# Kernel optimization log

Hardware: AMD Instinct MI355X
Metric: run time of the kernel (lower is better)

Reference implementation:

```python
import jax, jax.numpy as jnp
import numpy as np

G = 20000          # num_genes
B = 256            # batch_size
NNZ = 640000       # sparse adjacency nonzeros (avg degree 32)
K = 2              # PPR iterations
ALPHA = 0.1
NUM_CLASS = 33


def _spmm(rows, cols, vals, x):
    # y = A @ x with A sparse COO [G, G], x dense [G, B]
    return jax.ops.segment_sum(vals[:, None] * x[cols], rows, num_segments=G)


def setup_inputs() -> dict:
    key = jax.random.key(0)
    ks = jax.random.split(key, 18)
    inp = {
        "x_sample": jax.random.normal(ks[0], (B * G,), jnp.float32),
        "x_TF": jax.random.normal(ks[1], (B * G,), jnp.float32),
        "adj_rows": jax.random.randint(ks[2], (NNZ,), 0, G, jnp.int32),
        "adj_cols": jax.random.randint(ks[3], (NNZ,), 0, G, jnp.int32),
        "adj_vals": jax.random.uniform(ks[4], (NNZ,), jnp.float32) / 32.0,
        "adjT_rows": jax.random.randint(ks[5], (NNZ,), 0, G, jnp.int32),
        "adjT_cols": jax.random.randint(ks[6], (NNZ,), 0, G, jnp.int32),
        "adjT_vals": jax.random.uniform(ks[7], (NNZ,), jnp.float32) / 32.0,
        # learned scalar affine params (torch.rand(1))
        "emb_mut": jax.random.uniform(ks[8], (1,), jnp.float32),
        "bias_mut": jax.random.uniform(ks[9], (1,), jnp.float32),
        "emb_exp": jax.random.uniform(ks[10], (1,), jnp.float32),
        "bias_exp": jax.random.uniform(ks[11], (1,), jnp.float32),
        # MLP params (torch Linear layout: W [out, in])
        "W1": jax.random.normal(ks[12], (1024, G), jnp.float32) * (1.0 / np.sqrt(G)),
        "b1": jnp.zeros((1024,), jnp.float32),
        "W2": jax.random.normal(ks[13], (128, 1024), jnp.float32) * (1.0 / 32.0),
        "b2": jnp.zeros((128,), jnp.float32),
        "W3": jax.random.normal(ks[14], (NUM_CLASS, 128), jnp.float32) * (1.0 / np.sqrt(128.0)),
        "b3": jnp.zeros((NUM_CLASS,), jnp.float32),
    }
    return inp


def reference(x_sample, x_TF, adj_rows, adj_cols, adj_vals,
              adjT_rows, adjT_cols, adjT_vals,
              emb_mut, bias_mut, emb_exp, bias_exp,
              W1, b1, W2, b2, W3, b3):
    # scalar affine embedding + relu
    emb_m = jax.nn.relu(emb_mut * x_sample + bias_mut)   # [B*G]
    emb_e = jax.nn.relu(emb_exp * x_TF + bias_exp)       # [B*G]
    xs = emb_m.reshape(B, G).T                            # [G, B]
    xt = emb_e.reshape(B, G).T                            # [G, B]
    hs, ht = xs, xt
    one_m_a = 1.0 - ALPHA
    for _ in range(K):
        xs = _spmm(adj_rows, adj_cols, adj_vals, one_m_a * xs)
        xt = _spmm(adjT_rows, adjT_cols, adjT_vals, one_m_a * xt)
    xs = xs + ALPHA * hs
    xt = xt + ALPHA * ht
    hadamard = (xs * xt).T                                # [B, G]
    h1 = jax.nn.relu(hadamard @ W1.T + b1)                # [B, 1024]
    h2 = jax.nn.relu(h1 @ W2.T + b2)                      # [B, 128]
    return h2 @ W3.T + b3                                 # [B, num_class]
```

## Files before the change

kernel.cpp:

```cpp
#include <hip/hip_runtime.h>
#include <hip/hip_fp16.h>

#define G_   20000
#define B_   256
#define NNZ_ 640000
#define KCH_ 640
#define NZ_  32
#define NBUK 157
#define BCAP 4608
#define EPB  4000

typedef float f4 __attribute__((ext_vector_type(4)));
typedef _Float16 h8 __attribute__((ext_vector_type(8)));

__global__ __launch_bounds__(256) void zero_kernel(unsigned int* p, int n) {
    int i = blockIdx.x * 256 + threadIdx.x;
    if (i < n) p[i] = 0u;
}

__global__ __launch_bounds__(256) void pad_kernel(int* pA, int* pB) {
    int t = threadIdx.x;
    pA[t] = 0; pB[t] = 0;
}

__global__ __launch_bounds__(256) void embed_kernel(
        const float* __restrict__ xsamp, const float* __restrict__ xtf,
        const float* __restrict__ em, const float* __restrict__ bm,
        const float* __restrict__ ee, const float* __restrict__ be,
        __half* __restrict__ X0s, __half* __restrict__ X0t) {
    __shared__ float lds[64][65];
    const int t  = threadIdx.x;
    const int gb = blockIdx.x * 64, bb = blockIdx.y * 64;
    const float a_m = em[0], c_m = bm[0], a_e = ee[0], c_e = be[0];
    const int gl = t & 63, brow0 = t >> 6;
    const int cl = t & 31, row0  = t >> 5;
    const int g_l = gb + gl;
#pragma unroll
    for (int r = 0; r < 16; r++) {
        int bl = brow0 + r * 4;
        float v = 0.f;
        if (g_l < G_) v = xsamp[(size_t)(bb + bl) * G_ + g_l];
        lds[bl][gl] = fmaxf(a_m * v + c_m, 0.f);
    }
    __syncthreads();
#pragma unroll
    for (int r = 0; r < 8; r++) {
        int gl2 = row0 + r * 8;
        int g = gb + gl2;
        if (g < G_) {
            __half2 hv = __floats2half2_rn(lds[cl * 2][gl2], lds[cl * 2 + 1][gl2]);
            *(__half2*)(X0s + (size_t)g * B_ + bb + cl * 2) = hv;
        }
    }
    __syncthreads();
#pragma unroll
    for (int r = 0; r < 16; r++) {
        int bl = brow0 + r * 4;
        float v = 0.f;
        if (g_l < G_) v = xtf[(size_t)(bb + bl) * G_ + g_l];
        lds[bl][gl] = fmaxf(a_e * v + c_e, 0.f);
    }
    __syncthreads();
#pragma unroll
    for (int r = 0; r < 8; r++) {
        int gl2 = row0 + r * 8;
        int g = gb + gl2;
        if (g < G_) {
            __half2 hv = __floats2half2_rn(lds[cl * 2][gl2], lds[cl * 2 + 1][gl2]);
            *(__half2*)(X0t + (size_t)g * B_ + bb + cl * 2) = hv;
        }
    }
}

__global__ __launch_bounds__(256) void binsort_kernel(
        const int* __restrict__ rA, const int* __restrict__ cA, const float* __restrict__ vA,
        const int* __restrict__ rB, const int* __restrict__ cB, const float* __restrict__ vB,
        int2* __restrict__ metaA, int* __restrict__ cntA,
        int2* __restrict__ metaB, int* __restrict__ cntB) {
    __shared__ int2 stage[EPB];
    __shared__ unsigned char bkid[EPB];
    __shared__ int hist[NBUK], lstart[NBUK], gbase[NBUK];
    const int t = threadIdx.x;
    const int base = blockIdx.x * EPB;
    const int* rows; const int* colsp; const float* valsp; int2* meta; int* cnt;
    if (blockIdx.y == 0) { rows = rA; colsp = cA; valsp = vA; meta = metaA; cnt = cntA; }
    else                 { rows = rB; colsp = cB; valsp = vB; meta = metaB; cnt = cntB; }

    for (int i = t; i < NBUK; i += 256) hist[i] = 0;
    __syncthreads();
    for (int i = t; i < EPB; i += 256)
        atomicAdd(&hist[rows[base + i] >> 7], 1);
    __syncthreads();
    if (t == 0) {
        int s = 0;
        for (int b = 0; b < NBUK; b++) { lstart[b] = s; s += hist[b]; }
    }
    __syncthreads();
    if (t < NBUK) hist[t] = lstart[t];
    __syncthreads();
    for (int i = t; i < EPB; i += 256) {
        int r = rows[base + i];
        int c = colsp[base + i];
        float v = valsp[base + i];
        int b = r >> 7;
        int p = atomicAdd(&hist[b], 1);
        stage[p] = make_int2(((r & 127) << 24) | (c * (B_ * 2)),
                             __float_as_int(0.9f * v));
        bkid[p] = (unsigned char)b;
    }
    __syncthreads();
    if (t < NBUK) gbase[t] = atomicAdd(&cnt[t], hist[t] - lstart[t]);
    __syncthreads();
    for (int i = t; i < EPB; i += 256) {
        int b = bkid[i];
        meta[(size_t)b * BCAP + gbase[b] + (i - lstart[b])] = stage[i];
    }
}

__global__ __launch_bounds__(256) void rowsort_kernel(
        const int2* __restrict__ metaA, const int* __restrict__ cntA,
        int2* __restrict__ sortedA, int* __restrict__ rpA,
        const int2* __restrict__ metaB, const int* __restrict__ cntB,
        int2* __restrict__ sortedB, int* __restrict__ rpB) {
    __shared__ int2 stage[BCAP];
    __shared__ int2 sorted[BCAP];
    __shared__ int carr[NBUK];
    __shared__ int hist[128], lstart[128];
    const int t = threadIdx.x;
    const int buk = blockIdx.x;
    const int2* meta; const int* cnt; int2* outp; int* rp;
    if (blockIdx.y == 0) { meta = metaA; cnt = cntA; outp = sortedA; rp = rpA; }
    else                 { meta = metaB; cnt = cntB; outp = sortedB; rp = rpB; }

    if (t < NBUK) carr[t] = cnt[t];
    if (t < 128) hist[t] = 0;
    __syncthreads();
    int bukStart = 0, nE = carr[buk];
    for (int b = 0; b < NBUK; b++) bukStart += (b < buk) ? carr[b] : 0;

    const int2* mp = meta + (size_t)buk * BCAP;
    for (int i = t; i < nE; i += 256) {
        int2 m = mp[i];
        stage[i] = m;
        atomicAdd(&hist[(unsigned)m.x >> 24], 1);
    }
    __syncthreads();
    if (t == 0) {
        int s = 0;
        for (int r = 0; r < 128; r++) { lstart[r] = s; s += hist[r]; }
    }
    __syncthreads();
    if (t < 128) hist[t] = lstart[t];
    __syncthreads();
    for (int i = t; i < nE; i += 256) {
        int2 m = stage[i];
        int r = (unsigned)m.x >> 24;
        int p = atomicAdd(&hist[r], 1);
        sorted[p] = make_int2(m.x & 0xFFFFFF, m.y);
    }
    __syncthreads();
    for (int i = t; i < nE; i += 256)
        outp[bukStart + i] = sorted[i];
    if (t < 128) {
        int g = buk * 128 + t;
        if (g < G_) rp[g] = bukStart + lstart[t];
    }
    if (buk == NBUK - 1 && t == 0) rp[G_] = bukStart + nE;
}

__global__ __launch_bounds__(256) void spmm_kernel(
        const int* __restrict__ rpA, const int2* __restrict__ metaA,
        const __half* __restrict__ xinA, __half* __restrict__ xoutA,
        const int* __restrict__ rpB, const int2* __restrict__ metaB,
        const __half* __restrict__ xinB, __half* __restrict__ xoutB) {
    const int bid   = blockIdx.x;
    const int combo = bid & 7;
    const int rowblk = bid >> 3;
    const int chunk = combo & 3;
    const int t = threadIdx.x;
    const int wave = t >> 6, lane = t & 63;
    const int half = lane >> 5, cl = lane & 31;
    const int g = rowblk * 8 + wave * 2 + half;
    const int loff = chunk * 128 + cl * 4;
    const int* rp; const int2* meta; const __half* xin; __half* xout;
    if (combo < 4) { rp = rpA; meta = metaA; xin = xinA; xout = xoutA; }
    else           { rp = rpB; meta = metaB; xin = xinB; xout = xoutB; }
    int beg = rp[g];
    int n   = rp[g + 1] - beg;
    int nother = __shfl_xor(n, 32);
    int nmax = n > nother ? n : nother;
    const char* xb = (const char*)xin + loff;
    float ax = 0.f, ay = 0.f;
    int e = 0;
    for (; e + 4 <= nmax; e += 4) {
        int2 m0 = meta[beg + e],     m1 = meta[beg + e + 1];
        int2 m2 = meta[beg + e + 2], m3 = meta[beg + e + 3];
        float v0 = (e + 0 < n) ? __int_as_float(m0.y) : 0.f;
        float v1 = (e + 1 < n) ? __int_as_float(m1.y) : 0.f;
        float v2 = (e + 2 < n) ? __int_as_float(m2.y) : 0.f;
        float v3 = (e + 3 < n) ? __int_as_float(m3.y) : 0.f;
        float2 x0 = __half22float2(*(const __half2*)(xb + m0.x));
        float2 x1 = __half22float2(*(const __half2*)(xb + m1.x));
        float2 x2 = __half22float2(*(const __half2*)(xb + m2.x));
        float2 x3 = __half22float2(*(const __half2*)(xb + m3.x));
        ax = fmaf(v0, x0.x, ax); ay = fmaf(v0, x0.y, ay);
        ax = fmaf(v1, x1.x, ax); ay = fmaf(v1, x1.y, ay);
        ax = fmaf(v2, x2.x, ax); ay = fmaf(v2, x2.y, ay);
        ax = fmaf(v3, x3.x, ax); ay = fmaf(v3, x3.y, ay);
    }
    for (; e < nmax; ++e) {
        int2 m = meta[beg + e];
        float v = (e < n) ? __int_as_float(m.y) : 0.f;
        float2 x = __half22float2(*(const __half2*)(xb + m.x));
        ax = fmaf(v, x.x, ax); ay = fmaf(v, x.y, ay);
    }
    *(__half2*)((char*)xout + (size_t)g * (B_ * 2) + loff) = __floats2half2_rn(ax, ay);
}

__global__ __launch_bounds__(256) void combine_kernel(
        const __half* __restrict__ X2s, const __half* __restrict__ X0s,
        const __half* __restrict__ X2t, const __half* __restrict__ X0t,
        __half* __restrict__ hadBK) {
    __shared__ float lds[64][65];
    const int t = threadIdx.x;
    const int gb = blockIdx.x * 64, bb = blockIdx.y * 64;
    const int cl = t & 31, row0 = t >> 5;
#pragma unroll
    for (int r = 0; r < 8; r++) {
        int gl = row0 + r * 8;
        int g = gb + gl;
        float px = 0.f, py = 0.f;
        if (g < G_) {
            size_t idx = (size_t)g * B_ + bb + cl * 2;
            float2 x2s = __half22float2(*(const __half2*)(X2s + idx));
            float2 x0s = __half22float2(*(const __half2*)(X0s + idx));
            float2 x2t = __half22float2(*(const __half2*)(X2t + idx));
            float2 x0t = __half22float2(*(const __half2*)(X0t + idx));
            px = (x2s.x + 0.1f * x0s.x) * (x2t.x + 0.1f * x0t.x);
            py = (x2s.y + 0.1f * x0s.y) * (x2t.y + 0.1f * x0t.y);
        }
        lds[gl][cl * 2]     = px;
        lds[gl][cl * 2 + 1] = py;
    }
    __syncthreads();
#pragma unroll
    for (int r = 0; r < 8; r++) {
        int bl = row0 + r * 8;
        int g0 = gb + cl * 2;
        if (g0 < G_) {
            __half2 hv = __floats2half2_rn(lds[cl * 2][bl], lds[cl * 2 + 1][bl]);
            *(__half2*)(hadBK + (size_t)(bb + bl) * G_ + g0) = hv;
        }
    }
}

__global__ __launch_bounds__(512) void gemm1_kernel(
        const __half* __restrict__ hadBK, const float* __restrict__ W1,
        float* __restrict__ part) {
    __shared__ _Float16 a_lds[256][40];
    __shared__ _Float16 b_lds[128][40];
    const int t = threadIdx.x;
    const int lane = t & 63, wid = t >> 6;
    const int wm = wid >> 1, wn = wid & 1;
    const int l15 = lane & 15, l4 = lane >> 4;
    const int ob = blockIdx.x * 128;
    const int kb = blockIdx.y * KCH_;
    int kend = kb + KCH_; if (kend > G_) kend = G_;
    const int nsteps = (kend - kb) >> 5;
    const int ar = t >> 1, ah = t & 1;
    const int br = t >> 2, bs = t & 3;
    const _Float16* hadH = (const _Float16*)hadBK;
    f4 acc[4][4] = {};
    for (int s = 0; s < nsteps; ++s) {
        const int k0 = kb + s * 32;
        {
            const _Float16* src = hadH + (size_t)ar * G_ + k0 + ah * 16;
            *(h8*)&a_lds[ar][ah * 16]     = *(const h8*)(src);
            *(h8*)&a_lds[ar][ah * 16 + 8] = *(const h8*)(src + 8);
        }
        {
            const float* src = W1 + (size_t)(ob + br) * G_ + k0 + bs * 8;
            f4 w0 = *(const f4*)src;
            f4 w1 = *(const f4*)(src + 4);
            h8 h;
            h[0] = (_Float16)w0[0]; h[1] = (_Float16)w0[1];
            h[2] = (_Float16)w0[2]; h[3] = (_Float16)w0[3];
            h[4] = (_Float16)w1[0]; h[5] = (_Float16)w1[1];
            h[6] = (_Float16)w1[2]; h[7] = (_Float16)w1[3];
            *(h8*)&b_lds[br][bs * 8] = h;
        }
        __syncthreads();
        h8 af[4], bf[4];
#pragma unroll
        for (int m = 0; m < 4; m++)
            af[m] = *(const h8*)&a_lds[wm * 64 + m * 16 + l15][l4 * 8];
#pragma unroll
        for (int n = 0; n < 4; n++)
            bf[n] = *(const h8*)&b_lds[wn * 64 + n * 16 + l15][l4 * 8];
#pragma unroll
        for (int m = 0; m < 4; m++)
#pragma unroll
            for (int n = 0; n < 4; n++)
                acc[m][n] = __builtin_amdgcn_mfma_f32_16x16x32_f16(
                    af[m], bf[n], acc[m][n], 0, 0, 0);
        __syncthreads();
    }
    const size_t zoff = (size_t)blockIdx.y * (B_ * 1024);
#pragma unroll
    for (int m = 0; m < 4; m++)
#pragma unroll
        for (int n = 0; n < 4; n++)
#pragma unroll
            for (int j = 0; j < 4; j++) {
                int b = wm * 64 + m * 16 + l4 * 4 + j;
                int o = ob + wn * 64 + n * 16 + l15;
                part[zoff + (size_t)b * 1024 + o] = acc[m][n][j];
            }
}

__global__ __launch_bounds__(256) void reduce_kernel(
        const float* __restrict__ part, const float* __restrict__ b1,
        float* __restrict__ h1) {
    int i = blockIdx.x * 256 + threadIdx.x;
    float s = 0.f;
#pragma unroll
    for (int z = 0; z < NZ_; z++) s += part[(size_t)z * 262144 + i];
    h1[i] = fmaxf(s + b1[i & 1023], 0.f);
}

__global__ __launch_bounds__(128) void gemm23_kernel(
        const float* __restrict__ h1, const float* __restrict__ W2,
        const float* __restrict__ b2, const float* __restrict__ W3,
        const float* __restrict__ b3, float* __restrict__ out) {
    __shared__ float h1row[1024];
    __shared__ float h2[128];
    const int b = blockIdx.x, t = threadIdx.x;
    *(f4*)&h1row[t * 4]       = *(const f4*)(h1 + (size_t)b * 1024 + t * 4);
    *(f4*)&h1row[512 + t * 4] = *(const f4*)(h1 + (size_t)b * 1024 + 512 + t * 4);
    __syncthreads();
    {
        float acc = b2[t];
        const f4* w  = (const f4*)(W2 + (size_t)t * 1024);
        const f4* hr = (const f4*)h1row;
        for (int k = 0; k < 256; k++) {
            f4 wv = w[k], hv = hr[k];
            acc += wv[0] * hv[0] + wv[1] * hv[1] + wv[2] * hv[2] + wv[3] * hv[3];
        }
        h2[t] = fmaxf(acc, 0.f);
    }
    __syncthreads();
    if (t < 33) {
        float acc = b3[t];
        const f4* w  = (const f4*)(W3 + (size_t)t * 128);
        const f4* hv = (const f4*)h2;
#pragma unroll
        for (int k = 0; k < 32; k++) {
            f4 a = w[k], x = hv[k];
            acc += a[0] * x[0] + a[1] * x[1] + a[2] * x[2] + a[3] * x[3];
        }
        out[b * 33 + t] = acc;
    }
}

extern "C" void kernel_launch(void* const* d_in, const int* in_sizes, int n_in,
                              void* d_out, int out_size, void* d_ws, size_t ws_size,
                              hipStream_t stream) {
    const float* x_sample  = (const float*)d_in[0];
    const float* x_TF      = (const float*)d_in[1];
    const int*   adj_rows  = (const int*)d_in[2];
    const int*   adj_cols  = (const int*)d_in[3];
    const float* adj_vals  = (const float*)d_in[4];
    const int*   adjT_rows = (const int*)d_in[5];
    const int*   adjT_cols = (const int*)d_in[6];
    const float* adjT_vals = (const float*)d_in[7];
    const float* emb_mut   = (const float*)d_in[8];
    const float* bias_mut  = (const float*)d_in[9];
    const float* emb_exp   = (const float*)d_in[10];
    const float* bias_exp  = (const float*)d_in[11];
    const float* W1 = (const float*)d_in[12];
    const float* b1 = (const float*)d_in[13];
    const float* W2 = (const float*)d_in[14];
    const float* b2 = (const float*)d_in[15];
    const float* W3 = (const float*)d_in[16];
    const float* b3 = (const float*)d_in[17];
    float* out = (float*)d_out;

    char* w = (char*)d_ws;
    auto alloc = [&](size_t bytes) {
        char* p = w; w += (bytes + 255) & ~(size_t)255; return p;
    };
    __half* X0s = (__half*)alloc(5120000 * 2);
    __half* X1s = (__half*)alloc(5120000 * 2);
    __half* X2s = (__half*)alloc(5120000 * 2);
    __half* X0t = (__half*)alloc(5120000 * 2);
    __half* X1t = (__half*)alloc(5120000 * 2);
    __half* X2t = (__half*)alloc(5120000 * 2);
    float*  part = (float*)alloc((size_t)NZ_ * 262144 * 4);
    float*  h1   = (float*)alloc(262144 * 4);
    int2*   metaA   = (int2*)alloc((size_t)NBUK * BCAP * 8);
    int2*   metaB   = (int2*)alloc((size_t)NBUK * BCAP * 8);
    int2*   sortedA = (int2*)alloc((size_t)(NNZ_ + 128) * 8);
    int2*   sortedB = (int2*)alloc((size_t)(NNZ_ + 128) * 8);
    int*    cnt   = (int*)alloc(2 * NBUK * 4);
    int*    cntA  = cnt;
    int*    cntB  = cnt + NBUK;
    int*    rpA   = (int*)alloc(20001 * 4);
    int*    rpB   = (int*)alloc(20001 * 4);
    __half* hadBK = X1s;

    zero_kernel<<<2, 256, 0, stream>>>((unsigned int*)cnt, 2 * NBUK);
    pad_kernel<<<1, 256, 0, stream>>>((int*)(sortedA + NNZ_), (int*)(sortedB + NNZ_));

    embed_kernel<<<dim3(313, 4), 256, 0, stream>>>(
        x_sample, x_TF, emb_mut, bias_mut, emb_exp, bias_exp, X0s, X0t);

    binsort_kernel<<<dim3(160, 2), 256, 0, stream>>>(
        adj_rows, adj_cols, adj_vals, adjT_rows, adjT_cols, adjT_vals,
        metaA, cntA, metaB, cntB);
    rowsort_kernel<<<dim3(NBUK, 2), 256, 0, stream>>>(
        metaA, cntA, sortedA, rpA, metaB, cntB, sortedB, rpB);

    spmm_kernel<<<20000, 256, 0, stream>>>(rpA, sortedA, X0s, X1s,
                                           rpB, sortedB, X0t, X1t);
    spmm_kernel<<<20000, 256, 0, stream>>>(rpA, sortedA, X1s, X2s,
                                           rpB, sortedB, X1t, X2t);

    combine_kernel<<<dim3(313, 4), 256, 0, stream>>>(X2s, X0s, X2t, X0t, hadBK);

    gemm1_kernel<<<dim3(8, NZ_), 512, 0, stream>>>(hadBK, W1, part);
    reduce_kernel<<<1024, 256, 0, stream>>>(part, b1, h1);
    gemm23_kernel<<<B_, 128, 0, stream>>>(h1, W2, b2, W3, b3, out);
}
```

Before: 474.5 us.

## Widen SpMM gathers to 4 halves per lane and prefetch GEMM1 tiles into registers

Each SpMM lane now gathers and accumulates 4 fp16 values (8 bytes) instead of 2. This halves the grid and the number of index/value metadata loads per output element, but each lane carries more live accumulators. GEMM1 now loads the next K-step's A and W1 tiles into registers while the MFMAs for the current step run, a register double-buffering scheme meant to hide global load latency. The padding-zero kernel is folded into the last rowsort block, removing one launch.

```diff
diff --git a/kernel.cpp b/kernel.cpp
--- a/kernel.cpp
+++ b/kernel.cpp
@@ -16,11 +16,6 @@
 __global__ __launch_bounds__(256) void zero_kernel(unsigned int* p, int n) {
     int i = blockIdx.x * 256 + threadIdx.x;
     if (i < n) p[i] = 0u;
-}
-
-__global__ __launch_bounds__(256) void pad_kernel(int* pA, int* pB) {
-    int t = threadIdx.x;
-    pA[t] = 0; pB[t] = 0;
 }
 
 __global__ __launch_bounds__(256) void embed_kernel(
@@ -165,7 +160,10 @@
         int g = buk * 128 + t;
         if (g < G_) rp[g] = bukStart + lstart[t];
     }
-    if (buk == NBUK - 1 && t == 0) rp[G_] = bukStart + nE;
+    if (buk == NBUK - 1) {
+        if (t == 0) rp[G_] = bukStart + nE;
+        if (t < 128) outp[NNZ_ + t] = make_int2(0, 0);
+    }
 }
 
 __global__ __launch_bounds__(256) void spmm_kernel(
@@ -173,24 +171,24 @@
         const __half* __restrict__ xinA, __half* __restrict__ xoutA,
         const int* __restrict__ rpB, const int2* __restrict__ metaB,
         const __half* __restrict__ xinB, __half* __restrict__ xoutB) {
-    const int bid   = blockIdx.x;
-    const int combo = bid & 7;
-    const int rowblk = bid >> 3;
-    const int chunk = combo & 3;
+    const int bid    = blockIdx.x;
+    const int combo  = bid & 3;
+    const int rowblk = bid >> 2;
+    const int chunk  = combo & 1;
     const int t = threadIdx.x;
     const int wave = t >> 6, lane = t & 63;
     const int half = lane >> 5, cl = lane & 31;
     const int g = rowblk * 8 + wave * 2 + half;
-    const int loff = chunk * 128 + cl * 4;
+    const int loff = chunk * 256 + cl * 8;
     const int* rp; const int2* meta; const __half* xin; __half* xout;
-    if (combo < 4) { rp = rpA; meta = metaA; xin = xinA; xout = xoutA; }
+    if (combo < 2) { rp = rpA; meta = metaA; xin = xinA; xout = xoutA; }
     else           { rp = rpB; meta = metaB; xin = xinB; xout = xoutB; }
     int beg = rp[g];
     int n   = rp[g + 1] - beg;
     int nother = __shfl_xor(n, 32);
     int nmax = n > nother ? n : nother;
     const char* xb = (const char*)xin + loff;
-    float ax = 0.f, ay = 0.f;
+    float a0 = 0.f, a1 = 0.f, a2 = 0.f, a3 = 0.f;
     int e = 0;
     for (; e + 4 <= nmax; e += 4) {
         int2 m0 = meta[beg + e],     m1 = meta[beg + e + 1];
@@ -199,22 +197,37 @@
         float v1 = (e + 1 < n) ? __int_as_float(m1.y) : 0.f;
         float v2 = (e + 2 < n) ? __int_as_float(m2.y) : 0.f;
         float v3 = (e + 3 < n) ? __int_as_float(m3.y) : 0.f;
-        float2 x0 = __half22float2(*(const __half2*)(xb + m0.x));
-        float2 x1 = __half22float2(*(const __half2*)(xb + m1.x));
-        float2 x2 = __half22float2(*(const __half2*)(xb + m2.x));
-        float2 x3 = __half22float2(*(const __half2*)(xb + m3.x));
-        ax = fmaf(v0, x0.x, ax); ay = fmaf(v0, x0.y, ay);
-        ax = fmaf(v1, x1.x, ax); ay = fmaf(v1, x1.y, ay);
-        ax = fmaf(v2, x2.x, ax); ay = fmaf(v2, x2.y, ay);
-        ax = fmaf(v3, x3.x, ax); ay = fmaf(v3, x3.y, ay);
+        uint2 r0 = *(const uint2*)(xb + m0.x);
+        uint2 r1 = *(const uint2*)(xb + m1.x);
+        uint2 r2 = *(const uint2*)(xb + m2.x);
+        uint2 r3 = *(const uint2*)(xb + m3.x);
+        float2 l0 = __half22float2(*(__half2*)&r0.x), h0 = __half22float2(*(__half2*)&r0.y);
+        float2 l1 = __half22float2(*(__half2*)&r1.x), h1 = __half22float2(*(__half2*)&r1.y);
+        float2 l2 = __half22float2(*(__half2*)&r2.x), h2 = __half22float2(*(__half2*)&r2.y);
+        float2 l3 = __half22float2(*(__half2*)&r3.x), h3 = __half22float2(*(__half2*)&r3.y);
+        a0 = fmaf(v0, l0.x, a0); a1 = fmaf(v0, l0.y, a1);
+        a2 = fmaf(v0, h0.x, a2); a3 = fmaf(v0, h0.y, a3);
+        a0 = fmaf(v1, l1.x, a0); a1 = fmaf(v1, l1.y, a1);
+        a2 = fmaf(v1, h1.x, a2); a3 = fmaf(v1, h1.y, a3);
+        a0 = fmaf(v2, l2.x, a0); a1 = fmaf(v2, l2.y, a1);
+        a2 = fmaf(v2, h2.x, a2); a3 = fmaf(v2, h2.y, a3);
+        a0 = fmaf(v3, l3.x, a0); a1 = fmaf(v3, l3.y, a1);
+        a2 = fmaf(v3, h3.x, a2); a3 = fmaf(v3, h3.y, a3);
     }
     for (; e < nmax; ++e) {
         int2 m = meta[beg + e];
         float v = (e < n) ? __int_as_float(m.y) : 0.f;
-        float2 x = __half22float2(*(const __half2*)(xb + m.x));
-        ax = fmaf(v, x.x, ax); ay = fmaf(v, x.y, ay);
-    }
-    *(__half2*)((char*)xout + (size_t)g * (B_ * 2) + loff) = __floats2half2_rn(ax, ay);
+        uint2 r = *(const uint2*)(xb + m.x);
+        float2 l = __half22float2(*(__half2*)&r.x), h = __half22float2(*(__half2*)&r.y);
+        a0 = fmaf(v, l.x, a0); a1 = fmaf(v, l.y, a1);
+        a2 = fmaf(v, h.x, a2); a3 = fmaf(v, h.y, a3);
+    }
+    __half2 o0 = __floats2half2_rn(a0, a1);
+    __half2 o1 = __floats2half2_rn(a2, a3);
+    uint2 ov;
+    ov.x = *(unsigned*)&o0;
+    ov.y = *(unsigned*)&o1;
+    *(uint2*)((char*)xout + (size_t)g * (B_ * 2) + loff) = ov;
 }
 
 __global__ __launch_bounds__(256) void combine_kernel(
@@ -270,26 +283,32 @@
     const int ar = t >> 1, ah = t & 1;
     const int br = t >> 2, bs = t & 3;
     const _Float16* hadH = (const _Float16*)hadBK;
+    const _Float16* asrc = hadH + (size_t)ar * G_ + ah * 16;
+    const float*    bsrc = W1 + (size_t)(ob + br) * G_ + bs * 8;
     f4 acc[4][4] = {};
+    h8 ra0 = *(const h8*)(asrc + kb);
+    h8 ra1 = *(const h8*)(asrc + kb + 8);
+    f4 rb0 = *(const f4*)(bsrc + kb);
+    f4 rb1 = *(const f4*)(bsrc + kb + 4);
     for (int s = 0; s < nsteps; ++s) {
-        const int k0 = kb + s * 32;
+        *(h8*)&a_lds[ar][ah * 16]     = ra0;
+        *(h8*)&a_lds[ar][ah * 16 + 8] = ra1;
         {
-            const _Float16* src = hadH + (size_t)ar * G_ + k0 + ah * 16;
-            *(h8*)&a_lds[ar][ah * 16]     = *(const h8*)(src);
-            *(h8*)&a_lds[ar][ah * 16 + 8] = *(const h8*)(src + 8);
-        }
-        {
-            const float* src = W1 + (size_t)(ob + br) * G_ + k0 + bs * 8;
-            f4 w0 = *(const f4*)src;
-            f4 w1 = *(const f4*)(src + 4);
             h8 h;
-            h[0] = (_Float16)w0[0]; h[1] = (_Float16)w0[1];
-            h[2] = (_Float16)w0[2]; h[3] = (_Float16)w0[3];
-            h[4] = (_Float16)w1[0]; h[5] = (_Float16)w1[1];
-            h[6] = (_Float16)w1[2]; h[7] = (_Float16)w1[3];
+            h[0] = (_Float16)rb0[0]; h[1] = (_Float16)rb0[1];
+            h[2] = (_Float16)rb0[2]; h[3] = (_Float16)rb0[3];
+            h[4] = (_Float16)rb1[0]; h[5] = (_Float16)rb1[1];
+            h[6] = (_Float16)rb1[2]; h[7] = (_Float16)rb1[3];
             *(h8*)&b_lds[br][bs * 8] = h;
         }
         __syncthreads();
+        if (s + 1 < nsteps) {
+            const int k1 = kb + (s + 1) * 32;
+            ra0 = *(const h8*)(asrc + k1);
+            ra1 = *(const h8*)(asrc + k1 + 8);
+            rb0 = *(const f4*)(bsrc + k1);
+            rb1 = *(const f4*)(bsrc + k1 + 4);
+        }
         h8 af[4], bf[4];
 #pragma unroll
         for (int m = 0; m < 4; m++)
@@ -409,7 +428,6 @@
     __half* hadBK = X1s;
 
     zero_kernel<<<2, 256, 0, stream>>>((unsigned int*)cnt, 2 * NBUK);
-    pad_kernel<<<1, 256, 0, stream>>>((int*)(sortedA + NNZ_), (int*)(sortedB + NNZ_));
 
     embed_kernel<<<dim3(313, 4), 256, 0, stream>>>(
         x_sample, x_TF, emb_mut, bias_mut, emb_exp, bias_exp, X0s, X0t);
@@ -420,9 +438,9 @@
     rowsort_kernel<<<dim3(NBUK, 2), 256, 0, stream>>>(
         metaA, cntA, sortedA, rpA, metaB, cntB, sortedB, rpB);
 
-    spmm_kernel<<<20000, 256, 0, stream>>>(rpA, sortedA, X0s, X1s,
+    spmm_kernel<<<10000, 256, 0, stream>>>(rpA, sortedA, X0s, X1s,
                                            rpB, sortedB, X0t, X1t);
-    spmm_kernel<<<20000, 256, 0, stream>>>(rpA, sortedA, X1s, X2s,
+    spmm_kernel<<<10000, 256, 0, stream>>>(rpA, sortedA, X1s, X2s,
                                            rpB, sortedB, X1t, X2t);
 
     combine_kernel<<<dim3(313, 4), 256, 0, stream>>>(X2s, X0s, X2t, X0t, hadBK);
```

After: 445.8 us. 6.0% less time.
